# Kernel optimization log

Measured on AMD Instinct MI355X. Metric: run time of the kernel, lower is better.

Reference implementation:

```python
import jax, jax.numpy as jnp
import numpy as np

NUM_HEADS = 16
NUM_GROUPS = 4
EPS = 1e-6


def _rope_tables(seq_len, head_dim):
    inv_freq = 1.0 / (10000.0 ** (jnp.arange(0, head_dim, 2, dtype=jnp.float32) / head_dim))
    t = jnp.arange(seq_len, dtype=jnp.float32)
    freqs = jnp.outer(t, inv_freq)  # [s, hd//2]
    return jnp.sin(freqs), jnp.cos(freqs)


def _apply_rope(x, sin, cos):
    # x: [b, s, h, hd]; sin/cos: [s, hd//2] -> broadcast over batch and heads
    sin = sin[None, :, None, :]
    cos = cos[None, :, None, :]
    x1 = x[..., ::2]
    x2 = x[..., 1::2]
    out1 = x1 * cos - x2 * sin
    out2 = x1 * sin + x2 * cos
    return jnp.stack([out1, out2], axis=-1).reshape(x.shape).astype(x.dtype)


def _rmsnorm(x, scale):
    var = jnp.mean(jnp.square(x), axis=-1, keepdims=True)
    return x * jax.lax.rsqrt(var + EPS) * scale


def setup_inputs() -> dict:
    key = jax.random.key(0)
    b, s, d = 16, 512, 2048
    hd = d // NUM_HEADS
    g = NUM_GROUPS
    ks = jax.random.split(key, 9)
    std = 0.02
    return {
        "x": jax.random.normal(ks[0], (b, s, d), dtype=jnp.float32),
        "Wq": jax.random.normal(ks[1], (d, d), dtype=jnp.float32) * std,
        "bq": jnp.zeros((d,), dtype=jnp.float32),
        "Wk": jax.random.normal(ks[2], (d, g * hd), dtype=jnp.float32) * std,
        "bk": jnp.zeros((g * hd,), dtype=jnp.float32),
        "Wv": jax.random.normal(ks[3], (d, g * hd), dtype=jnp.float32) * std,
        "bv": jnp.zeros((g * hd,), dtype=jnp.float32),
        "Wo": jax.random.normal(ks[4], (d, d), dtype=jnp.float32) * std,
        "bo": jnp.zeros((d,), dtype=jnp.float32),
        "q_norm_scale": jnp.ones((hd,), dtype=jnp.float32),
        "k_norm_scale": jnp.ones((hd,), dtype=jnp.float32),
    }


def reference(x, Wq, bq, Wk, bk, Wv, bv, Wo, bo, q_norm_scale, k_norm_scale):
    b, s, d = x.shape
    H, G = NUM_HEADS, NUM_GROUPS
    hd = d // H
    P = H // G  # queries per kv group
    inv_sqrt_hd = hd ** (-0.5)

    q = (x @ Wq + bq).reshape(b, s, H, hd)
    k = (x @ Wk + bk).reshape(b, s, G, hd)
    v = (x @ Wv + bv).reshape(b, s, G, hd)

    q = _rmsnorm(q, q_norm_scale)
    k = _rmsnorm(k, k_norm_scale)

    sin, cos = _rope_tables(s, hd)
    q = _apply_rope(q, sin, cos) * inv_sqrt_hd  # module pre-scales q
    k = _apply_rope(k, sin, cos)

    # GQA attention with causal mask; dot_product_attention applies an
    # additional 1/sqrt(hd) scale on top of the module's pre-scaling.
    qg = q.reshape(b, s, G, P, hd)
    logits = jnp.einsum("bsgph,btgh->bgpst", qg, k) * inv_sqrt_hd
    causal = jnp.tril(jnp.ones((s, s), dtype=bool))
    logits = jnp.where(causal[None, None, None, :, :], logits, jnp.finfo(logits.dtype).min)
    attn = jax.nn.softmax(logits, axis=-1)
    out = jnp.einsum("bgpst,btgh->bsgph", attn, v).reshape(b, s, d)
    return out @ Wo + bo
```

## Files before the change

### kernel.cpp

```cpp
#include <hip/hip_runtime.h>
#include <stdint.h>

typedef __attribute__((ext_vector_type(4))) float floatx4;
typedef __attribute__((ext_vector_type(8))) short short8;

#define BB 16
#define SS 512
#define DD 2048
#define HH_ 16
#define HD 128
#define GG 4
#define MM (BB*SS)
#define NQKV 3072

__device__ __forceinline__ unsigned short f2bf(float f){
  unsigned u = __builtin_bit_cast(unsigned, f);
  u += 0x7fffu + ((u >> 16) & 1u);
  return (unsigned short)(u >> 16);
}
__device__ __forceinline__ float bf2f_lo(unsigned d){
  return __builtin_bit_cast(float, d << 16);
}
__device__ __forceinline__ float bf2f_hi(unsigned d){
  return __builtin_bit_cast(float, d & 0xffff0000u);
}

__device__ __forceinline__ void async_copy16(const void* g, void* l){
  __builtin_amdgcn_global_load_lds((const __attribute__((address_space(1))) unsigned*)g,
                                   (__attribute__((address_space(3))) unsigned*)l,
                                   16, 0, 0);
}

__global__ __launch_bounds__(256) void cvt_x_kernel(const float* __restrict__ src,
                                                    unsigned short* __restrict__ dst, int n4){
  int i = blockIdx.x * 256 + threadIdx.x;
  if (i >= n4) return;
  float4 f = ((const float4*)src)[i];
  ushort4 o;
  o.x = f2bf(f.x); o.y = f2bf(f.y); o.z = f2bf(f.z); o.w = f2bf(f.w);
  ((ushort4*)dst)[i] = o;
}

__global__ void tr_cvt_kernel(const float* __restrict__ src, unsigned short* __restrict__ dst,
                              int R, int C){
  __shared__ float tile[32][33];
  int c0 = blockIdx.x * 32, r0 = blockIdx.y * 32;
  int tx = threadIdx.x, ty = threadIdx.y;
  #pragma unroll
  for (int j = 0; j < 32; j += 8)
    tile[ty + j][tx] = src[(size_t)(r0 + ty + j) * C + (c0 + tx)];
  __syncthreads();
  #pragma unroll
  for (int j = 0; j < 32; j += 8)
    dst[(size_t)(c0 + ty + j) * R + (r0 + tx)] = f2bf(tile[tx][ty + j]);
}

__global__ void bias_cat_kernel(const float* __restrict__ bq, const float* __restrict__ bk,
                                const float* __restrict__ bv, float* __restrict__ out){
  int i = blockIdx.x * 256 + threadIdx.x;
  if (i >= NQKV) return;
  out[i] = (i < 2048) ? bq[i] : (i < 2560 ? bk[i - 2048] : bv[i - 2560]);
}

template<bool OUT_BF16>
__global__ __launch_bounds__(256) void gemm_bt_kernel(
    const unsigned short* __restrict__ A,
    const unsigned short* __restrict__ Bt,
    void* __restrict__ Cout,
    const float* __restrict__ bias,
    int M, int N, int K, int ldc)
{
  __shared__ unsigned short sA[128 * 32];
  __shared__ unsigned short sB[128 * 32];
  const int tid  = threadIdx.x;
  const int wave = tid >> 6;
  const int lane = tid & 63;
  const int m0 = blockIdx.y * 128;
  const int n0 = blockIdx.x * 128;
  const int wm = (wave >> 1) * 64;
  const int wn = (wave & 1) * 64;

  floatx4 acc[4][4];
  #pragma unroll
  for (int i = 0; i < 4; i++)
    #pragma unroll
    for (int j = 0; j < 4; j++)
      acc[i][j] = (floatx4){0.f, 0.f, 0.f, 0.f};

  const int rA = 32 * wave + (lane >> 2);
  const int cH = (((lane & 3) ^ ((lane >> 3) & 3))) * 8;
  const unsigned short* gA0 = A  + (size_t)(m0 + rA)      * K + cH;
  const unsigned short* gA1 = A  + (size_t)(m0 + rA + 16) * K + cH;
  const unsigned short* gB0 = Bt + (size_t)(n0 + rA)      * K + cH;
  const unsigned short* gB1 = Bt + (size_t)(n0 + rA + 16) * K + cH;
  unsigned short* lA0 = &sA[wave * 1024];
  unsigned short* lA1 = &sA[wave * 1024 + 512];
  unsigned short* lB0 = &sB[wave * 1024];
  unsigned short* lB1 = &sB[wave * 1024 + 512];

  const int fOffBase = (lane & 15) * 32 + (((lane >> 4) ^ (((lane & 15) >> 1) & 3)) * 8);

  for (int k0 = 0; k0 < K; k0 += 32) {
    async_copy16(gA0 + k0, lA0);
    async_copy16(gA1 + k0, lA1);
    async_copy16(gB0 + k0, lB0);
    async_copy16(gB1 + k0, lB1);
    __syncthreads();

    short8 aF[4], bF[4];
    #pragma unroll
    for (int i = 0; i < 4; i++)
      aF[i] = *(const short8*)(&sA[(wm + i * 16) * 32 + fOffBase]);
    #pragma unroll
    for (int j = 0; j < 4; j++)
      bF[j] = *(const short8*)(&sB[(wn + j * 16) * 32 + fOffBase]);

    #pragma unroll
    for (int i = 0; i < 4; i++)
      #pragma unroll
      for (int j = 0; j < 4; j++)
        acc[i][j] = __builtin_amdgcn_mfma_f32_16x16x32_bf16(aF[i], bF[j], acc[i][j], 0, 0, 0);
    __syncthreads();
  }

  const int cr = (lane >> 4) * 4;
  const int cc = lane & 15;
  #pragma unroll
  for (int j = 0; j < 4; j++) {
    const int col = n0 + wn + j * 16 + cc;
    const float bval = bias[col];
    #pragma unroll
    for (int i = 0; i < 4; i++) {
      #pragma unroll
      for (int r = 0; r < 4; r++) {
        const int row = m0 + wm + i * 16 + cr + r;
        const float v = acc[i][j][r] + bval;
        if (OUT_BF16)
          ((unsigned short*)Cout)[(size_t)row * ldc + col] = f2bf(v);
        else
          ((float*)Cout)[(size_t)row * ldc + col] = v;
      }
    }
  }
}

__global__ __launch_bounds__(256) void norm_rope_kernel(
    unsigned short* __restrict__ qkv,
    const float* __restrict__ qs, const float* __restrict__ ks)
{
  const int wave = threadIdx.x >> 6, lane = threadIdx.x & 63;
  const int gw  = blockIdx.x * 4 + wave;
  const int row = gw / 20;
  const int hh  = gw % 20;
  const bool isq = hh < 16;

  unsigned* p = (unsigned*)(qkv + (size_t)row * NQKV + hh * 128) + lane;
  unsigned d = *p;
  float x1 = bf2f_lo(d), x2 = bf2f_hi(d);

  float ss = x1 * x1 + x2 * x2;
  #pragma unroll
  for (int off = 32; off; off >>= 1) ss += __shfl_xor(ss, off, 64);
  const float r = rsqrtf(ss * (1.f / 128.f) + 1e-6f);

  const float2 sc = ((const float2*)(isq ? qs : ks))[lane];
  float n1 = x1 * r * sc.x;
  float n2 = x2 * r * sc.y;

  const float t = (float)(row & (SS - 1));
  const float freq = __expf((float)lane * (-2.f / 128.f) * 9.21034037197618f);
  float sn, cs;
  __sincosf(t * freq, &sn, &cs);
  float o1 = n1 * cs - n2 * sn;
  float o2 = n1 * sn + n2 * cs;
  if (isq) { o1 *= (1.f / 128.f); o2 *= (1.f / 128.f); }

  *p = (unsigned)f2bf(o1) | ((unsigned)f2bf(o2) << 16);
}

__global__ void vtr_kernel(const unsigned short* __restrict__ qkv,
                           unsigned short* __restrict__ vt){
  __shared__ unsigned short tile[32][34];
  const int hd0 = blockIdx.x * 32, t0 = blockIdx.y * 32, bg = blockIdx.z;
  const int tx = threadIdx.x, ty = threadIdx.y;
  const int b = bg >> 2, g = bg & 3;
  const unsigned short* src = qkv + (size_t)b * SS * NQKV + 2560 + g * HD;
  #pragma unroll
  for (int j = 0; j < 32; j += 8)
    tile[ty + j][tx] = src[(size_t)(t0 + ty + j) * NQKV + hd0 + tx];
  __syncthreads();
  unsigned short* dst = vt + (size_t)bg * HD * SS;
  #pragma unroll
  for (int j = 0; j < 32; j += 8)
    dst[(size_t)(hd0 + ty + j) * SS + t0 + tx] = tile[tx][ty + j];
}

__global__ __launch_bounds__(256) void fattn_kernel(
    const unsigned short* __restrict__ qkv,
    const unsigned short* __restrict__ vtb,
    unsigned short* __restrict__ aout)
{
  __shared__ unsigned short sK[64 * 128];
  __shared__ unsigned short sV[128 * 64];
  __shared__ unsigned short sP[4][16 * 72];

  const int lane = threadIdx.x & 63, wave = threadIdx.x >> 6;
  const int quad = lane >> 4, col = lane & 15;
  const int idx = blockIdx.x;
  const int qb = 7 - (idx >> 8);
  const int bh = idx & 255;
  const int b = bh >> 4, h = bh & 15, g = h >> 2;

  const int qrow = qb * 64 + wave * 16 + col;
  const unsigned short* qg = qkv + ((size_t)(b * SS + qrow)) * NQKV + h * HD + quad * 8;
  short8 qf[4];
  #pragma unroll
  for (int c = 0; c < 4; ++c) qf[c] = *(const short8*)(qg + c * 32);

  const unsigned short* kg = qkv + (size_t)b * SS * NQKV + 2048 + g * HD;
  const unsigned short* vg = vtb + ((size_t)(b * GG + g)) * HD * SS;

  floatx4 acc_o[8];
  #pragma unroll
  for (int i = 0; i < 8; ++i) acc_o[i] = (floatx4){0.f, 0.f, 0.f, 0.f};
  float m[4] = {-INFINITY, -INFINITY, -INFINITY, -INFINITY};
  float l[4] = {0.f, 0.f, 0.f, 0.f};

  for (int kt = 0; kt <= qb; ++kt) {
    const int t0 = kt * 64;
    #pragma unroll
    for (int c = 0; c < 4; ++c) {
      const int ci = c * 4 + wave;
      { const int r  = ci * 4 + (lane >> 4);
        const int gl = (lane & 15) ^ (r & 15);
        async_copy16(kg + (size_t)(t0 + r) * NQKV + gl * 8, &sK[ci * 512 + lane * 8]); }
      { const int r  = ci * 8 + (lane >> 3);
        const int gl = (lane & 7) ^ (r & 7);
        async_copy16(vg + (size_t)r * SS + t0 + gl * 8, &sV[ci * 512 + lane * 8]); }
    }
    __syncthreads();

    floatx4 sc[4];
    #pragma unroll
    for (int s = 0; s < 4; ++s) sc[s] = (floatx4){0.f, 0.f, 0.f, 0.f};
    #pragma unroll
    for (int s = 0; s < 4; ++s) {
      const int trow = s * 16 + col;
      #pragma unroll
      for (int c = 0; c < 4; ++c) {
        const int p = (c * 4 + quad) ^ (trow & 15);
        const short8 kf = *(const short8*)(&sK[trow * 128 + p * 8]);
        sc[s] = __builtin_amdgcn_mfma_f32_16x16x32_bf16(qf[c], kf, sc[s], 0, 0, 0);
      }
    }

    if (kt == qb) {
      #pragma unroll
      for (int s = 0; s < 4; ++s)
        #pragma unroll
        for (int r = 0; r < 4; ++r)
          if (s * 16 + col > wave * 16 + quad * 4 + r) sc[s][r] = -1e30f;
    }

    float mx[4], alpha[4], lsum[4];
    #pragma unroll
    for (int r = 0; r < 4; ++r) {
      mx[r] = fmaxf(fmaxf(sc[0][r], sc[1][r]), fmaxf(sc[2][r], sc[3][r]));
      #pragma unroll
      for (int off = 8; off; off >>= 1) mx[r] = fmaxf(mx[r], __shfl_xor(mx[r], off, 16));
      mx[r] = fmaxf(mx[r], m[r]);
      alpha[r] = __expf(m[r] - mx[r]);
      m[r] = mx[r];
      lsum[r] = 0.f;
    }
    #pragma unroll
    for (int s = 0; s < 4; ++s)
      #pragma unroll
      for (int r = 0; r < 4; ++r) {
        const float p = __expf(sc[s][r] - m[r]);
        lsum[r] += p;
        sP[wave][(quad * 4 + r) * 72 + s * 16 + col] = f2bf(p);
      }
    #pragma unroll
    for (int r = 0; r < 4; ++r) {
      #pragma unroll
      for (int off = 8; off; off >>= 1) lsum[r] += __shfl_xor(lsum[r], off, 16);
      l[r] = l[r] * alpha[r] + lsum[r];
    }
    #pragma unroll
    for (int n = 0; n < 8; ++n)
      #pragma unroll
      for (int r = 0; r < 4; ++r) acc_o[n][r] *= alpha[r];

    __asm__ volatile("s_waitcnt lgkmcnt(0)" ::: "memory");

    short8 pf[2];
    #pragma unroll
    for (int kc = 0; kc < 2; ++kc)
      pf[kc] = *(const short8*)(&sP[wave][col * 72 + kc * 32 + quad * 8]);
    #pragma unroll
    for (int n = 0; n < 8; ++n) {
      const int hdrow = n * 16 + col;
      #pragma unroll
      for (int kc = 0; kc < 2; ++kc) {
        const int p = (kc * 4 + quad) ^ (hdrow & 7);
        const short8 vf = *(const short8*)(&sV[hdrow * 64 + p * 8]);
        acc_o[n] = __builtin_amdgcn_mfma_f32_16x16x32_bf16(pf[kc], vf, acc_o[n], 0, 0, 0);
      }
    }
    __syncthreads();
  }

  float inv[4];
  #pragma unroll
  for (int r = 0; r < 4; ++r) inv[r] = 1.f / l[r];
  unsigned short* ob = aout + ((size_t)(b * SS + qb * 64 + wave * 16)) * DD + h * HD;
  #pragma unroll
  for (int n = 0; n < 8; ++n)
    #pragma unroll
    for (int r = 0; r < 4; ++r)
      ob[(size_t)(quad * 4 + r) * DD + n * 16 + col] = f2bf(acc_o[n][r] * inv[r]);
}

extern "C" void kernel_launch(void* const* d_in, const int* in_sizes, int n_in,
                              void* d_out, int out_size, void* d_ws, size_t ws_size,
                              hipStream_t stream) {
  const float* x   = (const float*)d_in[0];
  const float* Wq  = (const float*)d_in[1];
  const float* bq  = (const float*)d_in[2];
  const float* Wk  = (const float*)d_in[3];
  const float* bk  = (const float*)d_in[4];
  const float* Wv  = (const float*)d_in[5];
  const float* bv  = (const float*)d_in[6];
  const float* Wo  = (const float*)d_in[7];
  const float* bo  = (const float*)d_in[8];
  const float* qns = (const float*)d_in[9];
  const float* kns = (const float*)d_in[10];

  char* ws = (char*)d_ws;
  unsigned short* xb    = (unsigned short*)(ws);
  unsigned short* vtb   = (unsigned short*)(ws);
  unsigned short* WqkvT = (unsigned short*)(ws + 33554432);
  unsigned short* WoT   = (unsigned short*)(ws + 46137344);
  float*          bqkv  = (float*)         (ws + 54525952);
  unsigned short* qkv   = (unsigned short*)(ws + 54538240);
  unsigned short* aout  = (unsigned short*)(ws + 104869888);

  dim3 tb(32, 8);
  cvt_x_kernel<<<16384, 256, 0, stream>>>(x, xb, MM * DD / 4);
  tr_cvt_kernel<<<dim3(64, 64), tb, 0, stream>>>(Wq, WqkvT, 2048, 2048);
  tr_cvt_kernel<<<dim3(16, 64), tb, 0, stream>>>(Wk, WqkvT + (size_t)2048 * 2048, 2048, 512);
  tr_cvt_kernel<<<dim3(16, 64), tb, 0, stream>>>(Wv, WqkvT + (size_t)2560 * 2048, 2048, 512);
  tr_cvt_kernel<<<dim3(64, 64), tb, 0, stream>>>(Wo, WoT, 2048, 2048);
  bias_cat_kernel<<<12, 256, 0, stream>>>(bq, bk, bv, bqkv);

  gemm_bt_kernel<true><<<dim3(24, 64), 256, 0, stream>>>(xb, WqkvT, qkv, bqkv,
                                                         MM, NQKV, DD, NQKV);
  norm_rope_kernel<<<40960, 256, 0, stream>>>(qkv, qns, kns);
  vtr_kernel<<<dim3(4, 16, 64), tb, 0, stream>>>(qkv, vtb);
  fattn_kernel<<<2048, 256, 0, stream>>>(qkv, vtb, aout);
  gemm_bt_kernel<false><<<dim3(16, 64), 256, 0, stream>>>(aout, WoT, d_out, bo,
                                                          MM, DD, DD, DD);
  (void)in_sizes; (void)n_in; (void)out_size; (void)ws_size;
}
```

Before: 484.3 us.

## Use 32x32x16 MFMA with K=64 tiles in GEMM and merge prep launches

The GEMM kernel now uses 32x32x16 bf16 MFMA with 2x2 floatx16 accumulators per wave and a K-step of 64 with an 8-way XOR swizzle in LDS. This halves the number of barrier pairs and raises the arithmetic done per LDS fragment load. Separately, the five prep kernels (x conversion, weight transposes, bias concat) are merged into one launch, and norm/rope is merged with the V transpose, to cut launch overhead. The merge puts the transpose tiles' __syncthreads in divergent block ranges, which is safe because the branch is per-block.

```diff
diff --git a/kernel.cpp b/kernel.cpp
--- a/kernel.cpp
+++ b/kernel.cpp
@@ -2,6 +2,7 @@
 #include <stdint.h>
 
 typedef __attribute__((ext_vector_type(4))) float floatx4;
+typedef __attribute__((ext_vector_type(16))) float floatx16;
 typedef __attribute__((ext_vector_type(8))) short short8;
 
 #define BB 16
@@ -31,35 +32,56 @@
                                    16, 0, 0);
 }
 
-__global__ __launch_bounds__(256) void cvt_x_kernel(const float* __restrict__ src,
-                                                    unsigned short* __restrict__ dst, int n4){
-  int i = blockIdx.x * 256 + threadIdx.x;
-  if (i >= n4) return;
-  float4 f = ((const float4*)src)[i];
-  ushort4 o;
-  o.x = f2bf(f.x); o.y = f2bf(f.y); o.z = f2bf(f.z); o.w = f2bf(f.w);
-  ((ushort4*)dst)[i] = o;
-}
-
-__global__ void tr_cvt_kernel(const float* __restrict__ src, unsigned short* __restrict__ dst,
-                              int R, int C){
+#define PB_CVT   16384
+#define PB_TRQ   (PB_CVT + 4096)
+#define PB_TRK   (PB_TRQ + 1024)
+#define PB_TRV   (PB_TRK + 1024)
+#define PB_TRO   (PB_TRV + 4096)
+#define PB_ALL   (PB_TRO + 12)
+
+__global__ __launch_bounds__(256) void prep_kernel(
+    const float* __restrict__ x,
+    const float* __restrict__ Wq, const float* __restrict__ Wk,
+    const float* __restrict__ Wv, const float* __restrict__ Wo,
+    const float* __restrict__ bq, const float* __restrict__ bk,
+    const float* __restrict__ bv,
+    unsigned short* __restrict__ xb, unsigned short* __restrict__ WqkvT,
+    unsigned short* __restrict__ WoT, float* __restrict__ bqkv)
+{
   __shared__ float tile[32][33];
-  int c0 = blockIdx.x * 32, r0 = blockIdx.y * 32;
-  int tx = threadIdx.x, ty = threadIdx.y;
-  #pragma unroll
-  for (int j = 0; j < 32; j += 8)
-    tile[ty + j][tx] = src[(size_t)(r0 + ty + j) * C + (c0 + tx)];
-  __syncthreads();
-  #pragma unroll
-  for (int j = 0; j < 32; j += 8)
-    dst[(size_t)(c0 + ty + j) * R + (r0 + tx)] = f2bf(tile[tx][ty + j]);
-}
-
-__global__ void bias_cat_kernel(const float* __restrict__ bq, const float* __restrict__ bk,
-                                const float* __restrict__ bv, float* __restrict__ out){
-  int i = blockIdx.x * 256 + threadIdx.x;
-  if (i >= NQKV) return;
-  out[i] = (i < 2048) ? bq[i] : (i < 2560 ? bk[i - 2048] : bv[i - 2560]);
+  const int bid = blockIdx.x, tid = threadIdx.x;
+
+  if (bid < PB_CVT) {
+    const int i = bid * 256 + tid;
+    float4 f = ((const float4*)x)[i];
+    ushort4 o;
+    o.x = f2bf(f.x); o.y = f2bf(f.y); o.z = f2bf(f.z); o.w = f2bf(f.w);
+    ((ushort4*)xb)[i] = o;
+    return;
+  }
+  if (bid < PB_TRO) {
+    const float* src; unsigned short* dst; int R, C, b2;
+    if (bid < PB_TRQ)      { src = Wq; dst = WqkvT;                          R = 2048; C = 2048; b2 = bid - PB_CVT; }
+    else if (bid < PB_TRK) { src = Wk; dst = WqkvT + (size_t)2048 * 2048;    R = 2048; C = 512;  b2 = bid - PB_TRQ; }
+    else if (bid < PB_TRV) { src = Wv; dst = WqkvT + (size_t)2560 * 2048;    R = 2048; C = 512;  b2 = bid - PB_TRK; }
+    else                   { src = Wo; dst = WoT;                            R = 2048; C = 2048; b2 = bid - PB_TRV; }
+    const int nbx = C >> 5;
+    const int c0 = (b2 % nbx) * 32, r0 = (b2 / nbx) * 32;
+    const int tx = tid & 31, ty = tid >> 5;
+    #pragma unroll
+    for (int j = 0; j < 32; j += 8)
+      tile[ty + j][tx] = src[(size_t)(r0 + ty + j) * C + (c0 + tx)];
+    __syncthreads();
+    #pragma unroll
+    for (int j = 0; j < 32; j += 8)
+      dst[(size_t)(c0 + ty + j) * R + (r0 + tx)] = f2bf(tile[tx][ty + j]);
+    return;
+  }
+  {
+    const int i = (bid - PB_TRO) * 256 + tid;
+    if (i < NQKV)
+      bqkv[i] = (i < 2048) ? bq[i] : (i < 2560 ? bk[i - 2048] : bv[i - 2560]);
+  }
 }
 
 template<bool OUT_BF16>
@@ -70,8 +92,8 @@
     const float* __restrict__ bias,
     int M, int N, int K, int ldc)
 {
-  __shared__ unsigned short sA[128 * 32];
-  __shared__ unsigned short sB[128 * 32];
+  __shared__ unsigned short sA[128 * 64];
+  __shared__ unsigned short sB[128 * 64];
   const int tid  = threadIdx.x;
   const int wave = tid >> 6;
   const int lane = tid & 63;
@@ -80,61 +102,59 @@
   const int wm = (wave >> 1) * 64;
   const int wn = (wave & 1) * 64;
 
-  floatx4 acc[4][4];
-  #pragma unroll
-  for (int i = 0; i < 4; i++)
-    #pragma unroll
-    for (int j = 0; j < 4; j++)
-      acc[i][j] = (floatx4){0.f, 0.f, 0.f, 0.f};
-
-  const int rA = 32 * wave + (lane >> 2);
-  const int cH = (((lane & 3) ^ ((lane >> 3) & 3))) * 8;
-  const unsigned short* gA0 = A  + (size_t)(m0 + rA)      * K + cH;
-  const unsigned short* gA1 = A  + (size_t)(m0 + rA + 16) * K + cH;
-  const unsigned short* gB0 = Bt + (size_t)(n0 + rA)      * K + cH;
-  const unsigned short* gB1 = Bt + (size_t)(n0 + rA + 16) * K + cH;
-  unsigned short* lA0 = &sA[wave * 1024];
-  unsigned short* lA1 = &sA[wave * 1024 + 512];
-  unsigned short* lB0 = &sB[wave * 1024];
-  unsigned short* lB1 = &sB[wave * 1024 + 512];
-
-  const int fOffBase = (lane & 15) * 32 + (((lane >> 4) ^ (((lane & 15) >> 1) & 3)) * 8);
-
-  for (int k0 = 0; k0 < K; k0 += 32) {
-    async_copy16(gA0 + k0, lA0);
-    async_copy16(gA1 + k0, lA1);
-    async_copy16(gB0 + k0, lB0);
-    async_copy16(gB1 + k0, lB1);
-    __syncthreads();
-
-    short8 aF[4], bF[4];
-    #pragma unroll
-    for (int i = 0; i < 4; i++)
-      aF[i] = *(const short8*)(&sA[(wm + i * 16) * 32 + fOffBase]);
-    #pragma unroll
-    for (int j = 0; j < 4; j++)
-      bF[j] = *(const short8*)(&sB[(wn + j * 16) * 32 + fOffBase]);
-
-    #pragma unroll
-    for (int i = 0; i < 4; i++)
-      #pragma unroll
-      for (int j = 0; j < 4; j++)
-        acc[i][j] = __builtin_amdgcn_mfma_f32_16x16x32_bf16(aF[i], bF[j], acc[i][j], 0, 0, 0);
-    __syncthreads();
-  }
-
-  const int cr = (lane >> 4) * 4;
-  const int cc = lane & 15;
-  #pragma unroll
-  for (int j = 0; j < 4; j++) {
-    const int col = n0 + wn + j * 16 + cc;
+  floatx16 acc[2][2];
+  #pragma unroll
+  for (int i = 0; i < 2; i++)
+    #pragma unroll
+    for (int j = 0; j < 2; j++)
+      #pragma unroll
+      for (int r = 0; r < 16; r++) acc[i][j][r] = 0.f;
+
+  const int sglog = (lane & 7) ^ ((lane >> 3) & 7);
+  const unsigned short* gA = A  + (size_t)(m0 + 32 * wave + (lane >> 3)) * K + sglog * 8;
+  const unsigned short* gB = Bt + (size_t)(n0 + 32 * wave + (lane >> 3)) * K + sglog * 8;
+  unsigned short* lA = &sA[32 * wave * 64 + lane * 8];
+  unsigned short* lB = &sB[32 * wave * 64 + lane * 8];
+
+  for (int k0 = 0; k0 < K; k0 += 64) {
+    #pragma unroll
+    for (int c = 0; c < 4; ++c) {
+      async_copy16(gA + (size_t)c * 8 * K + k0, lA + c * 512);
+      async_copy16(gB + (size_t)c * 8 * K + k0, lB + c * 512);
+    }
+    __syncthreads();
+
+    #pragma unroll
+    for (int kh = 0; kh < 4; ++kh) {
+      const int slot = (kh * 2 + (lane >> 5)) ^ (lane & 7);
+      short8 aF[2], bF[2];
+      #pragma unroll
+      for (int i = 0; i < 2; ++i)
+        aF[i] = *(const short8*)(&sA[(wm + i * 32 + (lane & 31)) * 64 + slot * 8]);
+      #pragma unroll
+      for (int j = 0; j < 2; ++j)
+        bF[j] = *(const short8*)(&sB[(wn + j * 32 + (lane & 31)) * 64 + slot * 8]);
+      #pragma unroll
+      for (int i = 0; i < 2; ++i)
+        #pragma unroll
+        for (int j = 0; j < 2; ++j)
+          acc[i][j] = __builtin_amdgcn_mfma_f32_32x32x16_bf16(aF[i], bF[j], acc[i][j], 0, 0, 0);
+    }
+    __syncthreads();
+  }
+
+  const int cc = lane & 31;
+  const int rb = 4 * (lane >> 5);
+  #pragma unroll
+  for (int j = 0; j < 2; j++) {
+    const int col = n0 + wn + j * 32 + cc;
     const float bval = bias[col];
     #pragma unroll
-    for (int i = 0; i < 4; i++) {
-      #pragma unroll
-      for (int r = 0; r < 4; r++) {
-        const int row = m0 + wm + i * 16 + cr + r;
-        const float v = acc[i][j][r] + bval;
+    for (int i = 0; i < 2; i++) {
+      #pragma unroll
+      for (int reg = 0; reg < 16; reg++) {
+        const int row = m0 + wm + i * 32 + (reg & 3) + 8 * (reg >> 2) + rb;
+        const float v = acc[i][j][reg] + bval;
         if (OUT_BF16)
           ((unsigned short*)Cout)[(size_t)row * ldc + col] = f2bf(v);
         else
@@ -144,55 +164,60 @@
   }
 }
 
-__global__ __launch_bounds__(256) void norm_rope_kernel(
+__global__ __launch_bounds__(256) void norm_vtr_kernel(
     unsigned short* __restrict__ qkv,
-    const float* __restrict__ qs, const float* __restrict__ ks)
+    const float* __restrict__ qs, const float* __restrict__ ks,
+    unsigned short* __restrict__ vt)
 {
-  const int wave = threadIdx.x >> 6, lane = threadIdx.x & 63;
-  const int gw  = blockIdx.x * 4 + wave;
-  const int row = gw / 20;
-  const int hh  = gw % 20;
-  const bool isq = hh < 16;
-
-  unsigned* p = (unsigned*)(qkv + (size_t)row * NQKV + hh * 128) + lane;
-  unsigned d = *p;
-  float x1 = bf2f_lo(d), x2 = bf2f_hi(d);
-
-  float ss = x1 * x1 + x2 * x2;
-  #pragma unroll
-  for (int off = 32; off; off >>= 1) ss += __shfl_xor(ss, off, 64);
-  const float r = rsqrtf(ss * (1.f / 128.f) + 1e-6f);
-
-  const float2 sc = ((const float2*)(isq ? qs : ks))[lane];
-  float n1 = x1 * r * sc.x;
-  float n2 = x2 * r * sc.y;
-
-  const float t = (float)(row & (SS - 1));
-  const float freq = __expf((float)lane * (-2.f / 128.f) * 9.21034037197618f);
-  float sn, cs;
-  __sincosf(t * freq, &sn, &cs);
-  float o1 = n1 * cs - n2 * sn;
-  float o2 = n1 * sn + n2 * cs;
-  if (isq) { o1 *= (1.f / 128.f); o2 *= (1.f / 128.f); }
-
-  *p = (unsigned)f2bf(o1) | ((unsigned)f2bf(o2) << 16);
-}
-
-__global__ void vtr_kernel(const unsigned short* __restrict__ qkv,
-                           unsigned short* __restrict__ vt){
-  __shared__ unsigned short tile[32][34];
-  const int hd0 = blockIdx.x * 32, t0 = blockIdx.y * 32, bg = blockIdx.z;
-  const int tx = threadIdx.x, ty = threadIdx.y;
-  const int b = bg >> 2, g = bg & 3;
-  const unsigned short* src = qkv + (size_t)b * SS * NQKV + 2560 + g * HD;
-  #pragma unroll
-  for (int j = 0; j < 32; j += 8)
-    tile[ty + j][tx] = src[(size_t)(t0 + ty + j) * NQKV + hd0 + tx];
-  __syncthreads();
-  unsigned short* dst = vt + (size_t)bg * HD * SS;
-  #pragma unroll
-  for (int j = 0; j < 32; j += 8)
-    dst[(size_t)(hd0 + ty + j) * SS + t0 + tx] = tile[tx][ty + j];
+  __shared__ unsigned short tileV[32][34];
+  const int bid = blockIdx.x, tid = threadIdx.x;
+
+  if (bid < 40960) {
+    const int wave = tid >> 6, lane = tid & 63;
+    const int gw  = bid * 4 + wave;
+    const int row = gw / 20;
+    const int hh  = gw % 20;
+    const bool isq = hh < 16;
+
+    unsigned* p = (unsigned*)(qkv + (size_t)row * NQKV + hh * 128) + lane;
+    unsigned d = *p;
+    float x1 = bf2f_lo(d), x2 = bf2f_hi(d);
+
+    float ss = x1 * x1 + x2 * x2;
+    #pragma unroll
+    for (int off = 32; off; off >>= 1) ss += __shfl_xor(ss, off, 64);
+    const float r = rsqrtf(ss * (1.f / 128.f) + 1e-6f);
+
+    const float2 sc = ((const float2*)(isq ? qs : ks))[lane];
+    float n1 = x1 * r * sc.x;
+    float n2 = x2 * r * sc.y;
+
+    const float t = (float)(row & (SS - 1));
+    const float freq = __expf((float)lane * (-2.f / 128.f) * 9.21034037197618f);
+    float sn, cs;
+    __sincosf(t * freq, &sn, &cs);
+    float o1 = n1 * cs - n2 * sn;
+    float o2 = n1 * sn + n2 * cs;
+    if (isq) { o1 *= (1.f / 128.f); o2 *= (1.f / 128.f); }
+
+    *p = (unsigned)f2bf(o1) | ((unsigned)f2bf(o2) << 16);
+    return;
+  }
+  {
+    const int b2 = bid - 40960;
+    const int hd0 = (b2 & 3) * 32, t0 = ((b2 >> 2) & 15) * 32, bg = b2 >> 6;
+    const int tx = tid & 31, ty = tid >> 5;
+    const int b = bg >> 2, g = bg & 3;
+    const unsigned short* src = qkv + (size_t)b * SS * NQKV + 2560 + g * HD;
+    #pragma unroll
+    for (int j = 0; j < 32; j += 8)
+      tileV[ty + j][tx] = src[(size_t)(t0 + ty + j) * NQKV + hd0 + tx];
+    __syncthreads();
+    unsigned short* dst = vt + (size_t)bg * HD * SS;
+    #pragma unroll
+    for (int j = 0; j < 32; j += 8)
+      dst[(size_t)(hd0 + ty + j) * SS + t0 + tx] = tileV[tx][ty + j];
+  }
 }
 
 __global__ __launch_bounds__(256) void fattn_kernel(
@@ -346,18 +371,11 @@
   unsigned short* qkv   = (unsigned short*)(ws + 54538240);
   unsigned short* aout  = (unsigned short*)(ws + 104869888);
 
-  dim3 tb(32, 8);
-  cvt_x_kernel<<<16384, 256, 0, stream>>>(x, xb, MM * DD / 4);
-  tr_cvt_kernel<<<dim3(64, 64), tb, 0, stream>>>(Wq, WqkvT, 2048, 2048);
-  tr_cvt_kernel<<<dim3(16, 64), tb, 0, stream>>>(Wk, WqkvT + (size_t)2048 * 2048, 2048, 512);
-  tr_cvt_kernel<<<dim3(16, 64), tb, 0, stream>>>(Wv, WqkvT + (size_t)2560 * 2048, 2048, 512);
-  tr_cvt_kernel<<<dim3(64, 64), tb, 0, stream>>>(Wo, WoT, 2048, 2048);
-  bias_cat_kernel<<<12, 256, 0, stream>>>(bq, bk, bv, bqkv);
-
+  prep_kernel<<<PB_ALL, 256, 0, stream>>>(x, Wq, Wk, Wv, Wo, bq, bk, bv,
+                                          xb, WqkvT, WoT, bqkv);
   gemm_bt_kernel<true><<<dim3(24, 64), 256, 0, stream>>>(xb, WqkvT, qkv, bqkv,
                                                          MM, NQKV, DD, NQKV);
-  norm_rope_kernel<<<40960, 256, 0, stream>>>(qkv, qns, kns);
-  vtr_kernel<<<dim3(4, 16, 64), tb, 0, stream>>>(qkv, vtb);
+  norm_vtr_kernel<<<45056, 256, 0, stream>>>(qkv, qns, kns, vtb);
   fattn_kernel<<<2048, 256, 0, stream>>>(qkv, vtb, aout);
   gemm_bt_kernel<false><<<dim3(16, 64), 256, 0, stream>>>(aout, WoT, d_out, bo,
                                                           MM, DD, DD, DD);
```

After: 441.5 us. 1.1x faster.
